# Kernel optimization log

Hardware: AMD Instinct MI355X
Metric: run time of the kernel (lower is better)

## Reference

```python
import jax, jax.numpy as jnp
import numpy as np

UNITS = 512
GROUPS = 32
EPS = 1e-5


def group_norm(x, w, b, groups=GROUPS, eps=EPS):
    B, C, H, W = x.shape
    xg = x.reshape(B, groups, C // groups, H, W)
    mean = xg.mean(axis=(2, 3, 4), keepdims=True)
    var = ((xg - mean) ** 2).mean(axis=(2, 3, 4), keepdims=True)
    xg = (xg - mean) * jax.lax.rsqrt(var + eps)
    return xg.reshape(B, C, H, W) * w[None, :, None, None] + b[None, :, None, None]


def conv1x1(x, w, b):
    # w: [out_ch, in_ch], b: [out_ch]
    return jnp.einsum('oc,bchw->bohw', w, x) + b[None, :, None, None]


def setup_inputs() -> dict:
    key = jax.random.key(0)
    ks = jax.random.split(key, 11)
    C = UNITS
    s = 1.0 / np.sqrt(C)
    return {
        'x': jax.random.normal(ks[0], (16, C, 64, 64), dtype=jnp.float32),
        'gn_w': jnp.ones((C,), dtype=jnp.float32),
        'gn_b': jnp.zeros((C,), dtype=jnp.float32),
        'wq': jax.random.normal(ks[1], (C, C), dtype=jnp.float32) * s,
        'bq': jnp.zeros((C,), dtype=jnp.float32),
        'wk': jax.random.normal(ks[2], (C, C), dtype=jnp.float32) * s,
        'bk': jnp.zeros((C,), dtype=jnp.float32),
        'wv': jax.random.normal(ks[3], (C, C), dtype=jnp.float32) * s,
        'bv': jnp.zeros((C,), dtype=jnp.float32),
        'wp': jax.random.normal(ks[4], (C, C), dtype=jnp.float32) * s,
        'bp': jnp.zeros((C,), dtype=jnp.float32),
    }


def reference(x, gn_w, gn_b, wq, bq, wk, bk, wv, bv, wp, bp):
    B, C, H, W = x.shape
    g = GROUPS
    xn = group_norm(x, gn_w, gn_b)
    q = conv1x1(xn, wq, bq).reshape(B, g, C // g, H * W)
    k = conv1x1(xn, wk, bk).reshape(B, g, C // g, H * W)
    v = conv1x1(xn, wv, bv).reshape(B, g, C // g, H * W)
    # channel attention: scores over per-group channel dims, spatial contracted
    attn = jnp.einsum('bgci,bgdi->bgcd', q, k) / jnp.sqrt(jnp.float32(C))
    attn = jax.nn.softmax(attn, axis=-1)
    out = jnp.einsum('bgcd,bgdi->bgci', attn, v).reshape(B, C, H, W)
    # NB: original adds proj(out) to out (not a residual to the input)
    return out + conv1x1(out, wp, bp)
```

## Files before the change

kernel.cpp:

```cpp
#include <hip/hip_runtime.h>

typedef __attribute__((ext_vector_type(8))) short bf16x8;
typedef __attribute__((ext_vector_type(4))) float f32x4;
typedef __attribute__((ext_vector_type(8))) unsigned short us8;
typedef unsigned short u16;
typedef unsigned int u32;

__device__ __forceinline__ u16 f2bf(float f){
  u32 u = __builtin_bit_cast(u32, f);
  u32 r = (u + 0x7fffu + ((u >> 16) & 1u)) >> 16;
  return (u16)r;
}

#define ASYNC_CP16(gp, lp) __builtin_amdgcn_global_load_lds( \
    (__attribute__((address_space(1))) void*)(gp), \
    (__attribute__((address_space(3))) void*)(lp), 16, 0, 0)

__device__ const int d_rt[10] = {0,0,0,0,1,1,1,2,2,3};
__device__ const int d_ct[10] = {0,1,2,3,1,2,3,2,3,3};

__global__ __launch_bounds__(256) void k_stats(const float* __restrict__ x,
    const float* __restrict__ gnw, const float* __restrict__ gnb,
    u16* __restrict__ xb, float* __restrict__ a, float* __restrict__ cv,
    float* __restrict__ sx)
{
  int b = blockIdx.x >> 5;
  int g = blockIdx.x & 31;
  int tid = threadIdx.x;
  int cl = tid >> 4;
  int l16 = tid & 15;
  int c = g * 16 + cl;
  const float* xp = x + ((long)(b * 512 + c)) * 4096;
  u16* xbp = xb + ((long)(b * 512 + c)) * 4096;
  float s = 0.f, sq = 0.f;
  for (int it = 0; it < 64; ++it) {
    int i4 = it * 16 + l16;
    float4 v = *(const float4*)(xp + i4 * 4);
    s  += v.x + v.y + v.z + v.w;
    sq += v.x * v.x + v.y * v.y + v.z * v.z + v.w * v.w;
    ushort4 o;
    o.x = f2bf(v.x); o.y = f2bf(v.y); o.z = f2bf(v.z); o.w = f2bf(v.w);
    *(ushort4*)(xbp + i4 * 4) = o;
  }
  for (int off = 8; off; off >>= 1) { s += __shfl_xor(s, off); sq += __shfl_xor(sq, off); }
  __shared__ float chS[16], chQ[16];
  if (l16 == 0) { chS[cl] = s; chQ[cl] = sq; }
  __syncthreads();
  if (tid < 16) {
    float S = 0.f, Q = 0.f;
    for (int j = 0; j < 16; ++j) { S += chS[j]; Q += chQ[j]; }
    float mean = S * (1.f / 65536.f);
    float var  = Q * (1.f / 65536.f) - mean * mean;
    float rs = rsqrtf(var + 1e-5f);
    int cc = g * 16 + tid;
    float av = gnw[cc] * rs;
    a[b * 512 + cc]  = av;
    cv[b * 512 + cc] = gnb[cc] - mean * av;
    sx[b * 512 + cc] = chS[tid];
  }
}

__global__ __launch_bounds__(256) void k_wconv(const float* __restrict__ wq,
    const float* __restrict__ wp, u16* __restrict__ wqb, u16* __restrict__ wpI)
{
  int i = blockIdx.x * 256 + threadIdx.x;
  wqb[i] = f2bf(wq[i]);
  float add = ((i >> 9) == (i & 511)) ? 1.f : 0.f;
  wpI[i] = f2bf(wp[i] + add);
}

__global__ __launch_bounds__(256) void k_transpose(const u16* __restrict__ xb,
                                                   u16* __restrict__ xT)
{
  __shared__ u16 t[64][72];
  int i0 = blockIdx.x * 64, e0 = blockIdx.y * 64, b = blockIdx.z;
  int tid = threadIdx.x;
  #pragma unroll
  for (int p = 0; p < 2; ++p) {
    int task = p * 256 + tid;
    int er = task >> 3, ic = (task & 7) * 8;
    us8 v = *(const us8*)(xb + ((long)(b * 512 + e0 + er)) * 4096 + i0 + ic);
    #pragma unroll
    for (int j = 0; j < 8; ++j) t[ic + j][er] = v[j];
  }
  __syncthreads();
  #pragma unroll
  for (int p = 0; p < 2; ++p) {
    int task = p * 256 + tid;
    int ir = task >> 3, ec = (task & 7) * 8;
    us8 w = *(const us8*)&t[ir][ec];
    *(us8*)(xT + ((long)(b * 4096 + i0 + ir)) * 512 + e0 + ec) = w;
  }
}

#define SWZ_RD(row16, chunk) ((((chunk) ^ ((row16) & 7)) << 3))

__global__ __launch_bounds__(256) void k_gram_split(const u16* __restrict__ xb,
                                                    float* __restrict__ part)
{
  __shared__ u16 As[2][128 * 64];
  __shared__ u16 Bs[2][128 * 64];
  const int tid = threadIdx.x;
  const int wave = tid >> 6, lane = tid & 63;
  const int tile = blockIdx.x % 10, split = blockIdx.x / 10;
  const int b = blockIdx.y;
  const int tm = d_rt[tile] * 128, tn = d_ct[tile] * 128;
  const u16* Xb = xb + (long)b * 512 * 4096;
  const int wm = (wave >> 1) << 6, wn = (wave & 1) << 6;
  const int l15 = lane & 15, l4 = lane >> 4;

  f32x4 acc[4][4];
  f32x4 z = {0.f, 0.f, 0.f, 0.f};
  #pragma unroll
  for (int fm = 0; fm < 4; ++fm)
    #pragma unroll
    for (int fn = 0; fn < 4; ++fn) acc[fm][fn] = z;

  const int qa = wave * 4;
  const int srow = lane >> 3;
  const int k0 = split * 1024;
  const int NT = 16;

  auto STAGE = [&](int buf, int kt) {
    #pragma unroll
    for (int j = 0; j < 4; ++j) {
      int q = qa + j;
      int row = q * 8 + srow;
      int gcol = kt + (((lane & 7) ^ (row & 7)) << 3);
      ASYNC_CP16(Xb + (long)(tm + row) * 4096 + gcol, &As[buf][q * 512]);
      ASYNC_CP16(Xb + (long)(tn + row) * 4096 + gcol, &Bs[buf][q * 512]);
    }
  };

  STAGE(0, k0);
  int cur = 0;
  for (int t = 0; t < NT; ++t) {
    if (t + 1 < NT) {
      STAGE(cur ^ 1, k0 + (t + 1) * 64);
      asm volatile("s_waitcnt vmcnt(8)" ::: "memory");
    } else {
      asm volatile("s_waitcnt vmcnt(0)" ::: "memory");
    }
    __builtin_amdgcn_s_barrier();
    __builtin_amdgcn_sched_barrier(0);
    #pragma unroll
    for (int kk = 0; kk < 2; ++kk) {
      bf16x8 af[4], bfr[4];
      #pragma unroll
      for (int f = 0; f < 4; ++f) {
        af[f]  = *(const bf16x8*)&As[cur][(wm + f * 16 + l15) * 64 +
                                          SWZ_RD(l15, l4 + kk * 4)];
        bfr[f] = *(const bf16x8*)&Bs[cur][(wn + f * 16 + l15) * 64 +
                                          SWZ_RD(l15, l4 + kk * 4)];
      }
      #pragma unroll
      for (int fm = 0; fm < 4; ++fm)
        #pragma unroll
        for (int fn = 0; fn < 4; ++fn)
          acc[fm][fn] = __builtin_amdgcn_mfma_f32_16x16x32_bf16(
              bfr[fn], af[fm], acc[fm][fn], 0, 0, 0);
    }
    __builtin_amdgcn_sched_barrier(0);
    __builtin_amdgcn_s_barrier();
    cur ^= 1;
  }

  float* pp = part + ((((long)split * 16 + b) * 10 + tile) << 14);
  #pragma unroll
  for (int fm = 0; fm < 4; ++fm) {
    const int row = wm + fm * 16 + l15;
    #pragma unroll
    for (int fn = 0; fn < 4; ++fn) {
      const int col = wn + fn * 16 + l4 * 4;
      *(f32x4*)&pp[row * 128 + col] = acc[fm][fn];
    }
  }
}

__global__ __launch_bounds__(512) void k_gram_reduce(
    const float* __restrict__ part, const float* __restrict__ a,
    u16* __restrict__ Gp)
{
  const int tile = blockIdx.x, b = blockIdx.y;
  const int tmt = d_rt[tile], tnt = d_ct[tile];
  const int tm = tmt * 128, tn = tnt * 128;
  const int tid = threadIdx.x;
  __shared__ u16 t[128][130];
  const float* p0 = part + (((long)b * 10 + tile) << 14);
  const long ss = (long)16 * 10 * 16384;
  u16* Gb = Gp + (long)b * 262144;
  const float acol = a[b * 512 + tn + (tid & 127)];
  for (int chunk = 0; chunk < 32; ++chunk) {
    int idx = chunk * 512 + tid;
    int row = idx >> 7, col = idx & 127;
    float v = p0[idx] + p0[idx + ss] + p0[idx + 2 * ss] + p0[idx + 3 * ss];
    v *= a[b * 512 + tm + row] * acol;
    u16 bf = f2bf(v);
    Gb[(tm + row) * 512 + tn + col] = bf;
    t[row][col] = bf;
  }
  if (tmt != tnt) {
    __syncthreads();
    for (int chunk = 0; chunk < 32; ++chunk) {
      int idx = chunk * 512 + tid;
      int row = idx >> 7, col = idx & 127;
      Gb[(tn + row) * 512 + tm + col] = t[col][row];
    }
  }
}

template<int EPI>
__global__ __launch_bounds__(256) void k_ntgemm64(
    const u16* __restrict__ A, long sA, int lda,
    const u16* __restrict__ B, long sB, int ldb,
    float* __restrict__ fout, long sF, int ldf,
    u16* __restrict__ bout, long sO, int ldo_,
    const float* __restrict__ ascale)
{
  __shared__ u16 As[2][64 * 64];
  __shared__ u16 Bs[2][64 * 64];
  const int tid = threadIdx.x;
  const int wave = tid >> 6, lane = tid & 63;
  const int b = blockIdx.y;
  const int tm = (blockIdx.x >> 3) * 64, tn = (blockIdx.x & 7) * 64;
  const u16* Ab = A + sA * b;
  const u16* Bb = B + sB * b;
  const int wm = (wave >> 1) << 5, wn = (wave & 1) << 5;
  const int l15 = lane & 15, l4 = lane >> 4;

  f32x4 acc[2][2];
  f32x4 z = {0.f, 0.f, 0.f, 0.f};
  #pragma unroll
  for (int fm = 0; fm < 2; ++fm)
    #pragma unroll
    for (int fn = 0; fn < 2; ++fn) acc[fm][fn] = z;

  const int qa = wave * 2;
  const int srow = lane >> 3;
  const int NT = 8;

  auto STAGE = [&](int buf, int kt) {
    #pragma unroll
    for (int j = 0; j < 2; ++j) {
      int q = qa + j;
      int row = q * 8 + srow;
      int gcol = kt + (((lane & 7) ^ (row & 7)) << 3);
      ASYNC_CP16(Ab + (long)(tm + row) * lda + gcol, &As[buf][q * 512]);
      ASYNC_CP16(Bb + (long)(tn + row) * ldb + gcol, &Bs[buf][q * 512]);
    }
  };

  STAGE(0, 0);
  int cur = 0;
  for (int t = 0; t < NT; ++t) {
    if (t + 1 < NT) {
      STAGE(cur ^ 1, (t + 1) * 64);
      asm volatile("s_waitcnt vmcnt(4)" ::: "memory");
    } else {
      asm volatile("s_waitcnt vmcnt(0)" ::: "memory");
    }
    __builtin_amdgcn_s_barrier();
    __builtin_amdgcn_sched_barrier(0);
    #pragma unroll
    for (int kk = 0; kk < 2; ++kk) {
      bf16x8 af[2], bfr[2];
      #pragma unroll
      for (int f = 0; f < 2; ++f) {
        af[f]  = *(const bf16x8*)&As[cur][(wm + f * 16 + l15) * 64 +
                                          SWZ_RD(l15, l4 + kk * 4)];
        bfr[f] = *(const bf16x8*)&Bs[cur][(wn + f * 16 + l15) * 64 +
                                          SWZ_RD(l15, l4 + kk * 4)];
      }
      #pragma unroll
      for (int fm = 0; fm < 2; ++fm)
        #pragma unroll
        for (int fn = 0; fn < 2; ++fn)
          acc[fm][fn] = __builtin_amdgcn_mfma_f32_16x16x32_bf16(
              bfr[fn], af[fm], acc[fm][fn], 0, 0, 0);
    }
    __builtin_amdgcn_sched_barrier(0);
    __builtin_amdgcn_s_barrier();
    cur ^= 1;
  }

  #pragma unroll
  for (int fm = 0; fm < 2; ++fm) {
    const int row = tm + wm + fm * 16 + l15;
    #pragma unroll
    for (int fn = 0; fn < 2; ++fn) {
      const int col = tn + wn + fn * 16 + l4 * 4;
      f32x4 v = acc[fm][fn];
      if (EPI == 1) {
        *(f32x4*)&fout[sF * b + (long)row * ldf + col] = v;
      } else {
        f32x4 sc = *(const f32x4*)&ascale[b * 512 + col];
        ushort4 o;
        o.x = f2bf(v[0] * sc[0]); o.y = f2bf(v[1] * sc[1]);
        o.z = f2bf(v[2] * sc[2]); o.w = f2bf(v[3] * sc[3]);
        *(ushort4*)&bout[sO * b + (long)row * ldo_ + col] = o;
      }
    }
  }
}

__global__ __launch_bounds__(512, 2) void k_final(
    const u16* __restrict__ W3, const u16* __restrict__ xT,
    const float* __restrict__ cadd, float* __restrict__ out)
{
  __shared__ u16 As[2][256 * 64];
  __shared__ u16 Bs[2][256 * 64];
  const int tid = threadIdx.x;
  const int wave = tid >> 6, lane = tid & 63;
  const int b = blockIdx.y;
  const int bxx = blockIdx.x;
  const int mi = (bxx >> 3) & 1;
  const int ni = (bxx & 7) | ((bxx >> 4) << 3);
  const int tm = mi * 256, tn = ni * 256;
  const u16* Ab = W3 + (long)b * 262144;
  const u16* Bb = xT + (long)b * 4096 * 512;
  const int wmA = (wave >> 2) * 128, wnB = (wave & 3) * 64;
  const int l15 = lane & 15, l4 = lane >> 4;

  f32x4 acc[8][4];
  f32x4 z = {0.f, 0.f, 0.f, 0.f};
  #pragma unroll
  for (int fm = 0; fm < 8; ++fm)
    #pragma unroll
    for (int fn = 0; fn < 4; ++fn) acc[fm][fn] = z;

  const int qa = wave * 4;
  const int srow = lane >> 3;
  const int NT = 8;

  auto STAGE = [&](int buf, int kt) {
    #pragma unroll
    for (int j = 0; j < 4; ++j) {
      int q = qa + j;
      int row = q * 8 + srow;
      int gcol = kt + (((lane & 7) ^ (row & 7)) << 3);
      ASYNC_CP16(Ab + (long)(tm + row) * 512 + gcol, &As[buf][q * 512]);
      ASYNC_CP16(Bb + (long)(tn + row) * 512 + gcol, &Bs[buf][q * 512]);
    }
  };

  STAGE(0, 0);
  int cur = 0;
  for (int t = 0; t < NT; ++t) {
    if (t + 1 < NT) {
      STAGE(cur ^ 1, (t + 1) * 64);
      asm volatile("s_waitcnt vmcnt(8)" ::: "memory");
    } else {
      asm volatile("s_waitcnt vmcnt(0)" ::: "memory");
    }
    __builtin_amdgcn_s_barrier();
    __builtin_amdgcn_sched_barrier(0);
    #pragma unroll
    for (int kk = 0; kk < 2; ++kk) {
      bf16x8 af[8], bfr[4];
      #pragma unroll
      for (int f = 0; f < 8; ++f)
        af[f]  = *(const bf16x8*)&As[cur][(wmA + f * 16 + l15) * 64 +
                                          SWZ_RD(l15, l4 + kk * 4)];
      #pragma unroll
      for (int f = 0; f < 4; ++f)
        bfr[f] = *(const bf16x8*)&Bs[cur][(wnB + f * 16 + l15) * 64 +
                                          SWZ_RD(l15, l4 + kk * 4)];
      #pragma unroll
      for (int fm = 0; fm < 8; ++fm)
        #pragma unroll
        for (int fn = 0; fn < 4; ++fn)
          acc[fm][fn] = __builtin_amdgcn_mfma_f32_16x16x32_bf16(
              bfr[fn], af[fm], acc[fm][fn], 0, 0, 0);
    }
    __builtin_amdgcn_sched_barrier(0);
    __builtin_amdgcn_s_barrier();
    cur ^= 1;
  }

  float* ob = out + (long)b * 512 * 4096;
  #pragma unroll
  for (int fm = 0; fm < 8; ++fm) {
    const int row = tm + wmA + fm * 16 + l15;
    const float ca = cadd[b * 512 + row];
    #pragma unroll
    for (int fn = 0; fn < 4; ++fn) {
      const int col = tn + wnB + fn * 16 + l4 * 4;
      f32x4 v = acc[fm][fn];
      v[0] += ca; v[1] += ca; v[2] += ca; v[3] += ca;
      *(f32x4*)&ob[(long)row * 4096 + col] = v;
    }
  }
}

__global__ __launch_bounds__(256) void k_vec(
    const float* __restrict__ wq, const float* __restrict__ bq,
    const float* __restrict__ wk, const float* __restrict__ bk,
    const float* __restrict__ wv, const float* __restrict__ bv,
    const float* __restrict__ a, const float* __restrict__ cv,
    const float* __restrict__ sx,
    float* __restrict__ eq, float* __restrict__ uq, float* __restrict__ ek,
    float* __restrict__ uk, float* __restrict__ hv)
{
  int b = blockIdx.x / 5, which = blockIdx.x % 5;
  __shared__ float vec[512];
  int tid = threadIdx.x;
  for (int i = tid; i < 512; i += 256)
    vec[i] = (which == 1 || which == 3) ? a[b * 512 + i] * sx[b * 512 + i]
                                        : cv[b * 512 + i];
  __syncthreads();
  const float* W = (which < 2) ? wq : (which < 4) ? wk : wv;
  const float* bias = (which == 0) ? bq : (which == 2) ? bk : (which == 4) ? bv : nullptr;
  float* outp = (which == 0) ? eq : (which == 1) ? uq : (which == 2) ? ek
              : (which == 3) ? uk : hv;
  for (int c = tid; c < 512; c += 256) {
    const float* wr = W + (long)c * 512;
    float s2 = 0.f;
    for (int e = 0; e < 512; e += 4) {
      float4 w4 = *(const float4*)(wr + e);
      s2 += w4.x * vec[e] + w4.y * vec[e + 1] + w4.z * vec[e + 2] + w4.w * vec[e + 3];
    }
    if (bias) s2 += bias[c];
    outp[b * 512 + c] = s2;
  }
}

__global__ __launch_bounds__(256) void k_scores(
    const float* __restrict__ P,
    const float* __restrict__ wk, const float* __restrict__ wv,
    const float* __restrict__ eq, const float* __restrict__ uq,
    const float* __restrict__ ek, const float* __restrict__ uk,
    const float* __restrict__ hv,
    u16* __restrict__ UT, float* __restrict__ oc)
{
  int b = blockIdx.x >> 5, g = blockIdx.x & 31;
  int tid = threadIdx.x;
  __shared__ float Pl[16 * 516];
  __shared__ float Wl[16 * 516];
  __shared__ float at[16][16];

  const float* Pb = P + (long)b * 262144 + g * 16 * 512;
  for (int t = tid; t < 16 * 128; t += 256) {
    int r = t >> 7, q = t & 127;
    *(float4*)&Pl[r * 516 + q * 4] = *(const float4*)(Pb + r * 512 + q * 4);
  }
  const float* Wkb = wk + (long)g * 16 * 512;
  for (int t = tid; t < 16 * 128; t += 256) {
    int r = t >> 7, q = t & 127;
    *(float4*)&Wl[r * 516 + q * 4] = *(const float4*)(Wkb + r * 512 + q * 4);
  }
  __syncthreads();

  int c = tid >> 4, d = tid & 15;
  float s0 = 0.f;
  for (int e = 0; e < 512; e += 4) {
    float4 p4 = *(const float4*)&Pl[c * 516 + e];
    float4 w4 = *(const float4*)&Wl[d * 516 + e];
    s0 += p4.x * w4.x + p4.y * w4.y + p4.z * w4.z + p4.w * w4.w;
  }
  float eqc = eq[b * 512 + g * 16 + c], uqc = uq[b * 512 + g * 16 + c];
  float ekd = ek[b * 512 + g * 16 + d], ukd = uk[b * 512 + g * 16 + d];
  float s = (s0 + eqc * ukd + uqc * ekd + 4096.f * eqc * ekd) * 0.04419417382415922f;
  float m = s;
  for (int off = 8; off; off >>= 1) m = fmaxf(m, __shfl_xor(m, off));
  float p = expf(s - m);
  float sum = p;
  for (int off = 8; off; off >>= 1) sum += __shfl_xor(sum, off);
  at[c][d] = p / sum;
  __syncthreads();

  const float* Wvb = wv + (long)g * 16 * 512;
  for (int t = tid; t < 16 * 128; t += 256) {
    int r = t >> 7, q = t & 127;
    *(float4*)&Wl[r * 516 + q * 4] = *(const float4*)(Wvb + r * 512 + q * 4);
  }
  __syncthreads();

  for (int t = 0; t < 32; ++t) {
    int flat = t * 256 + tid;
    int cc = flat >> 9, e = flat & 511;
    float a2 = 0.f;
    #pragma unroll
    for (int dd = 0; dd < 16; ++dd) a2 += at[cc][dd] * Wl[dd * 516 + e];
    Pl[cc * 516 + e] = a2;
  }
  if (tid < 16) {
    float o2 = 0.f;
    #pragma unroll
    for (int dd = 0; dd < 16; ++dd) o2 += at[tid][dd] * hv[b * 512 + g * 16 + dd];
    oc[b * 512 + g * 16 + tid] = o2;
  }
  __syncthreads();
  for (int t = 0; t < 32; ++t) {
    int flat = t * 256 + tid;
    int cc = flat & 15, e = flat >> 4;
    UT[(long)b * 262144 + e * 512 + g * 16 + cc] = f2bf(Pl[cc * 516 + e]);
  }
}

__global__ __launch_bounds__(256) void k_c3(const float* __restrict__ wp,
    const float* __restrict__ bp, const float* __restrict__ oc,
    float* __restrict__ c3)
{
  int b = blockIdx.x >> 1;
  int o = (blockIdx.x & 1) * 256 + threadIdx.x;
  __shared__ float ov[512];
  for (int i = threadIdx.x; i < 512; i += 256) ov[i] = oc[b * 512 + i];
  __syncthreads();
  const float* wr = wp + (long)o * 512;
  float s = 0.f;
  for (int e = 0; e < 512; e += 4) {
    float4 w4 = *(const float4*)(wr + e);
    s += w4.x * ov[e] + w4.y * ov[e + 1] + w4.z * ov[e + 2] + w4.w * ov[e + 3];
  }
  c3[b * 512 + o] = oc[b * 512 + o] + s + bp[o];
}

extern "C" void kernel_launch(void* const* d_in, const int* in_sizes, int n_in,
                              void* d_out, int out_size, void* d_ws, size_t ws_size,
                              hipStream_t stream)
{
  (void)in_sizes; (void)n_in; (void)out_size; (void)ws_size;
  const float* x   = (const float*)d_in[0];
  const float* gnw = (const float*)d_in[1];
  const float* gnb = (const float*)d_in[2];
  const float* wq  = (const float*)d_in[3];
  const float* bq  = (const float*)d_in[4];
  const float* wk  = (const float*)d_in[5];
  const float* bk  = (const float*)d_in[6];
  const float* wv  = (const float*)d_in[7];
  const float* bv  = (const float*)d_in[8];
  const float* wp  = (const float*)d_in[9];
  const float* bp  = (const float*)d_in[10];
  float* out = (float*)d_out;

  char* ws = (char*)d_ws;
  u16* xT  = (u16*)ws;  ws += (size_t)16 * 4096 * 512 * 2;
  u16* Gp  = (u16*)ws;  ws += (size_t)16 * 512 * 512 * 2;
  float* P = (float*)ws; ws += (size_t)16 * 512 * 512 * 4;
  u16* UT  = (u16*)ws;  ws += (size_t)16 * 512 * 512 * 2;
  u16* W3  = (u16*)ws;  ws += (size_t)16 * 512 * 512 * 2;
  u16* wqb = (u16*)ws;  ws += (size_t)512 * 512 * 2;
  u16* wpI = (u16*)ws;  ws += (size_t)512 * 512 * 2;
  float* a  = (float*)ws; ws += 16 * 512 * 4;
  float* cv = (float*)ws; ws += 16 * 512 * 4;
  float* sx = (float*)ws; ws += 16 * 512 * 4;
  float* eq = (float*)ws; ws += 16 * 512 * 4;
  float* uq = (float*)ws; ws += 16 * 512 * 4;
  float* ek = (float*)ws; ws += 16 * 512 * 4;
  float* uk = (float*)ws; ws += 16 * 512 * 4;
  float* hv = (float*)ws; ws += 16 * 512 * 4;
  float* oc = (float*)ws; ws += 16 * 512 * 4;
  float* c3 = (float*)ws; ws += 16 * 512 * 4;

  u16* xb = (u16*)d_out;
  float* part = (float*)xT;

  k_stats<<<512, 256, 0, stream>>>(x, gnw, gnb, xb, a, cv, sx);
  k_wconv<<<1024, 256, 0, stream>>>(wq, wp, wqb, wpI);
  k_gram_split<<<dim3(40, 16), 256, 0, stream>>>(xb, part);
  k_gram_reduce<<<dim3(10, 16), 512, 0, stream>>>(part, a, Gp);
  k_transpose<<<dim3(64, 8, 16), 256, 0, stream>>>(xb, xT);
  k_vec<<<80, 256, 0, stream>>>(wq, bq, wk, bk, wv, bv, a, cv, sx,
                                eq, uq, ek, uk, hv);
  k_ntgemm64<1><<<dim3(64, 16), 256, 0, stream>>>(
      wqb, 0, 512, Gp, 262144, 512,
      P, 262144, 512, nullptr, 0, 0, nullptr);
  k_scores<<<512, 256, 0, stream>>>(P, wk, wv, eq, uq, ek, uk, hv, UT, oc);
  k_c3<<<32, 256, 0, stream>>>(wp, bp, oc, c3);
  k_ntgemm64<2><<<dim3(64, 16), 256, 0, stream>>>(
      wpI, 0, 512, UT, 262144, 512,
      nullptr, 0, 0, W3, 262144, 512, a);
  k_final<<<dim3(32, 16), 512, 0, stream>>>(W3, xT, c3, out);
}
```

Measured before the change: 281.2 us.

## Fuse weight conversion into stats kernel and shrink gram K-tile to 32

Folds the weight bf16 conversion into extra blocks of the stats kernel, removing one launch. Halves the gram_split K tile from 64 to 32 with 32 iterations and a 4-way swizzle, cutting LDS use and possibly raising occupancy at the cost of more barriers per K. Moves the partial-sum buffer into the output buffer after xb instead of aliasing xT, so the transpose can no longer collide with it.

New measurement: 285.8 us. About the same (+1.6%).

```diff
diff --git a/kernel.cpp b/kernel.cpp
--- a/kernel.cpp
+++ b/kernel.cpp
@@ -21,12 +21,20 @@
 
 __global__ __launch_bounds__(256) void k_stats(const float* __restrict__ x,
     const float* __restrict__ gnw, const float* __restrict__ gnb,
-    u16* __restrict__ xb, float* __restrict__ a, float* __restrict__ cv,
-    float* __restrict__ sx)
-{
+    const float* __restrict__ wq, const float* __restrict__ wp,
+    u16* __restrict__ xb, u16* __restrict__ wqb, u16* __restrict__ wpI,
+    float* __restrict__ a, float* __restrict__ cv, float* __restrict__ sx)
+{
+  int tid = threadIdx.x;
+  if (blockIdx.x >= 512) {
+    int i = (blockIdx.x - 512) * 256 + tid;
+    wqb[i] = f2bf(wq[i]);
+    float add = ((i >> 9) == (i & 511)) ? 1.f : 0.f;
+    wpI[i] = f2bf(wp[i] + add);
+    return;
+  }
   int b = blockIdx.x >> 5;
   int g = blockIdx.x & 31;
-  int tid = threadIdx.x;
   int cl = tid >> 4;
   int l16 = tid & 15;
   int c = g * 16 + cl;
@@ -60,15 +68,6 @@
   }
 }
 
-__global__ __launch_bounds__(256) void k_wconv(const float* __restrict__ wq,
-    const float* __restrict__ wp, u16* __restrict__ wqb, u16* __restrict__ wpI)
-{
-  int i = blockIdx.x * 256 + threadIdx.x;
-  wqb[i] = f2bf(wq[i]);
-  float add = ((i >> 9) == (i & 511)) ? 1.f : 0.f;
-  wpI[i] = f2bf(wp[i] + add);
-}
-
 __global__ __launch_bounds__(256) void k_transpose(const u16* __restrict__ xb,
                                                    u16* __restrict__ xT)
 {
@@ -98,8 +97,8 @@
 __global__ __launch_bounds__(256) void k_gram_split(const u16* __restrict__ xb,
                                                     float* __restrict__ part)
 {
-  __shared__ u16 As[2][128 * 64];
-  __shared__ u16 Bs[2][128 * 64];
+  __shared__ u16 As[2][128 * 32];
+  __shared__ u16 Bs[2][128 * 32];
   const int tid = threadIdx.x;
   const int wave = tid >> 6, lane = tid & 63;
   const int tile = blockIdx.x % 10, split = blockIdx.x / 10;
@@ -116,50 +115,45 @@
     #pragma unroll
     for (int fn = 0; fn < 4; ++fn) acc[fm][fn] = z;
 
-  const int qa = wave * 4;
-  const int srow = lane >> 3;
   const int k0 = split * 1024;
-  const int NT = 16;
+  const int NT = 32;
 
   auto STAGE = [&](int buf, int kt) {
     #pragma unroll
-    for (int j = 0; j < 4; ++j) {
-      int q = qa + j;
-      int row = q * 8 + srow;
-      int gcol = kt + (((lane & 7) ^ (row & 7)) << 3);
-      ASYNC_CP16(Xb + (long)(tm + row) * 4096 + gcol, &As[buf][q * 512]);
-      ASYNC_CP16(Xb + (long)(tn + row) * 4096 + gcol, &Bs[buf][q * 512]);
+    for (int l = 0; l < 2; ++l) {
+      int fbase = l * 256 + wave * 64;
+      int flat  = fbase + lane;
+      int row = flat >> 2, cseg = flat & 3;
+      int gcol = kt + ((cseg ^ (row & 3)) << 3);
+      ASYNC_CP16(Xb + (long)(tm + row) * 4096 + gcol, &As[buf][fbase * 8]);
+      ASYNC_CP16(Xb + (long)(tn + row) * 4096 + gcol, &Bs[buf][fbase * 8]);
     }
   };
 
   STAGE(0, k0);
   int cur = 0;
+  const int rswz = (l4 ^ (l15 & 3)) << 3;
   for (int t = 0; t < NT; ++t) {
     if (t + 1 < NT) {
-      STAGE(cur ^ 1, k0 + (t + 1) * 64);
-      asm volatile("s_waitcnt vmcnt(8)" ::: "memory");
+      STAGE(cur ^ 1, k0 + (t + 1) * 32);
+      asm volatile("s_waitcnt vmcnt(4)" ::: "memory");
     } else {
       asm volatile("s_waitcnt vmcnt(0)" ::: "memory");
     }
     __builtin_amdgcn_s_barrier();
     __builtin_amdgcn_sched_barrier(0);
-    #pragma unroll
-    for (int kk = 0; kk < 2; ++kk) {
-      bf16x8 af[4], bfr[4];
+    bf16x8 af[4], bfr[4];
+    #pragma unroll
+    for (int f = 0; f < 4; ++f) {
+      af[f]  = *(const bf16x8*)&As[cur][(wm + f * 16 + l15) * 32 + rswz];
+      bfr[f] = *(const bf16x8*)&Bs[cur][(wn + f * 16 + l15) * 32 + rswz];
+    }
+    #pragma unroll
+    for (int fm = 0; fm < 4; ++fm)
       #pragma unroll
-      for (int f = 0; f < 4; ++f) {
-        af[f]  = *(const bf16x8*)&As[cur][(wm + f * 16 + l15) * 64 +
-                                          SWZ_RD(l15, l4 + kk * 4)];
-        bfr[f] = *(const bf16x8*)&Bs[cur][(wn + f * 16 + l15) * 64 +
-                                          SWZ_RD(l15, l4 + kk * 4)];
-      }
-      #pragma unroll
-      for (int fm = 0; fm < 4; ++fm)
-        #pragma unroll
-        for (int fn = 0; fn < 4; ++fn)
-          acc[fm][fn] = __builtin_amdgcn_mfma_f32_16x16x32_bf16(
-              bfr[fn], af[fm], acc[fm][fn], 0, 0, 0);
-    }
+      for (int fn = 0; fn < 4; ++fn)
+        acc[fm][fn] = __builtin_amdgcn_mfma_f32_16x16x32_bf16(
+            bfr[fn], af[fm], acc[fm][fn], 0, 0, 0);
     __builtin_amdgcn_sched_barrier(0);
     __builtin_amdgcn_s_barrier();
     cur ^= 1;
@@ -553,10 +547,10 @@
   float* c3 = (float*)ws; ws += 16 * 512 * 4;
 
   u16* xb = (u16*)d_out;
-  float* part = (float*)xT;
-
-  k_stats<<<512, 256, 0, stream>>>(x, gnw, gnb, xb, a, cv, sx);
-  k_wconv<<<1024, 256, 0, stream>>>(wq, wp, wqb, wpI);
+  float* part = (float*)((char*)d_out + 67108864);
+
+  k_stats<<<1536, 256, 0, stream>>>(x, gnw, gnb, wq, wp, xb, wqb, wpI,
+                                    a, cv, sx);
   k_gram_split<<<dim3(40, 16), 256, 0, stream>>>(xb, part);
   k_gram_reduce<<<dim3(10, 16), 512, 0, stream>>>(part, a, Gp);
   k_transpose<<<dim3(64, 8, 16), 256, 0, stream>>>(xb, xT);
```

## Retile final GEMM to 128x128 tiles and fold weight conversion into stats

Applied to the files above, without the earlier changes.

The final output GEMM changes from 256x256 tiles with 512 threads and 8x4 MFMA fragments per wave to 128x128 tiles with 256 threads and 4x4 fragments, launched as 2048 blocks instead of 512. The aim is finer-grained parallelism and lower register and LDS pressure per block, traded against less data reuse per tile and more global loads. Separately, the weight bf16-conversion kernel is merged into the group-norm stats kernel as extra blocks, removing one launch. The Gram partial-sum buffer is moved to the upper half of the output buffer instead of aliasing xT.

After: 285.6 us. No clear change (+1.5%).

```diff
diff --git a/kernel.cpp b/kernel.cpp
--- a/kernel.cpp
+++ b/kernel.cpp
@@ -21,12 +21,20 @@
 
 __global__ __launch_bounds__(256) void k_stats(const float* __restrict__ x,
     const float* __restrict__ gnw, const float* __restrict__ gnb,
-    u16* __restrict__ xb, float* __restrict__ a, float* __restrict__ cv,
-    float* __restrict__ sx)
-{
+    const float* __restrict__ wq, const float* __restrict__ wp,
+    u16* __restrict__ xb, u16* __restrict__ wqb, u16* __restrict__ wpI,
+    float* __restrict__ a, float* __restrict__ cv, float* __restrict__ sx)
+{
+  int tid = threadIdx.x;
+  if (blockIdx.x >= 512) {
+    int i = (blockIdx.x - 512) * 256 + tid;
+    wqb[i] = f2bf(wq[i]);
+    float add = ((i >> 9) == (i & 511)) ? 1.f : 0.f;
+    wpI[i] = f2bf(wp[i] + add);
+    return;
+  }
   int b = blockIdx.x >> 5;
   int g = blockIdx.x & 31;
-  int tid = threadIdx.x;
   int cl = tid >> 4;
   int l16 = tid & 15;
   int c = g * 16 + cl;
@@ -58,15 +66,6 @@
     cv[b * 512 + cc] = gnb[cc] - mean * av;
     sx[b * 512 + cc] = chS[tid];
   }
-}
-
-__global__ __launch_bounds__(256) void k_wconv(const float* __restrict__ wq,
-    const float* __restrict__ wp, u16* __restrict__ wqb, u16* __restrict__ wpI)
-{
-  int i = blockIdx.x * 256 + threadIdx.x;
-  wqb[i] = f2bf(wq[i]);
-  float add = ((i >> 9) == (i & 511)) ? 1.f : 0.f;
-  wpI[i] = f2bf(wp[i] + add);
 }
 
 __global__ __launch_bounds__(256) void k_transpose(const u16* __restrict__ xb,
@@ -303,28 +302,26 @@
   }
 }
 
-__global__ __launch_bounds__(512, 2) void k_final(
+__global__ __launch_bounds__(256) void k_final(
     const u16* __restrict__ W3, const u16* __restrict__ xT,
     const float* __restrict__ cadd, float* __restrict__ out)
 {
-  __shared__ u16 As[2][256 * 64];
-  __shared__ u16 Bs[2][256 * 64];
+  __shared__ u16 As[2][128 * 64];
+  __shared__ u16 Bs[2][128 * 64];
   const int tid = threadIdx.x;
   const int wave = tid >> 6, lane = tid & 63;
   const int b = blockIdx.y;
-  const int bxx = blockIdx.x;
-  const int mi = (bxx >> 3) & 1;
-  const int ni = (bxx & 7) | ((bxx >> 4) << 3);
-  const int tm = mi * 256, tn = ni * 256;
+  const int tm = (blockIdx.x >> 5) * 128;
+  const int tn = (blockIdx.x & 31) * 128;
   const u16* Ab = W3 + (long)b * 262144;
   const u16* Bb = xT + (long)b * 4096 * 512;
-  const int wmA = (wave >> 2) * 128, wnB = (wave & 3) * 64;
+  const int wm = (wave >> 1) << 6, wn = (wave & 1) << 6;
   const int l15 = lane & 15, l4 = lane >> 4;
 
-  f32x4 acc[8][4];
+  f32x4 acc[4][4];
   f32x4 z = {0.f, 0.f, 0.f, 0.f};
   #pragma unroll
-  for (int fm = 0; fm < 8; ++fm)
+  for (int fm = 0; fm < 4; ++fm)
     #pragma unroll
     for (int fn = 0; fn < 4; ++fn) acc[fm][fn] = z;
 
@@ -356,17 +353,16 @@
     __builtin_amdgcn_sched_barrier(0);
     #pragma unroll
     for (int kk = 0; kk < 2; ++kk) {
-      bf16x8 af[8], bfr[4];
+      bf16x8 af[4], bfr[4];
       #pragma unroll
-      for (int f = 0; f < 8; ++f)
-        af[f]  = *(const bf16x8*)&As[cur][(wmA + f * 16 + l15) * 64 +
+      for (int f = 0; f < 4; ++f) {
+        af[f]  = *(const bf16x8*)&As[cur][(wm + f * 16 + l15) * 64 +
                                           SWZ_RD(l15, l4 + kk * 4)];
+        bfr[f] = *(const bf16x8*)&Bs[cur][(wn + f * 16 + l15) * 64 +
+                                          SWZ_RD(l15, l4 + kk * 4)];
+      }
       #pragma unroll
-      for (int f = 0; f < 4; ++f)
-        bfr[f] = *(const bf16x8*)&Bs[cur][(wnB + f * 16 + l15) * 64 +
-                                          SWZ_RD(l15, l4 + kk * 4)];
-      #pragma unroll
-      for (int fm = 0; fm < 8; ++fm)
+      for (int fm = 0; fm < 4; ++fm)
         #pragma unroll
         for (int fn = 0; fn < 4; ++fn)
           acc[fm][fn] = __builtin_amdgcn_mfma_f32_16x16x32_bf16(
@@ -379,12 +375,12 @@
 
   float* ob = out + (long)b * 512 * 4096;
   #pragma unroll
-  for (int fm = 0; fm < 8; ++fm) {
-    const int row = tm + wmA + fm * 16 + l15;
+  for (int fm = 0; fm < 4; ++fm) {
+    const int row = tm + wm + fm * 16 + l15;
     const float ca = cadd[b * 512 + row];
     #pragma unroll
     for (int fn = 0; fn < 4; ++fn) {
-      const int col = tn + wnB + fn * 16 + l4 * 4;
+      const int col = tn + wn + fn * 16 + l4 * 4;
       f32x4 v = acc[fm][fn];
       v[0] += ca; v[1] += ca; v[2] += ca; v[3] += ca;
       *(f32x4*)&ob[(long)row * 4096 + col] = v;
@@ -553,10 +549,10 @@
   float* c3 = (float*)ws; ws += 16 * 512 * 4;
 
   u16* xb = (u16*)d_out;
-  float* part = (float*)xT;
-
-  k_stats<<<512, 256, 0, stream>>>(x, gnw, gnb, xb, a, cv, sx);
-  k_wconv<<<1024, 256, 0, stream>>>(wq, wp, wqb, wpI);
+  float* part = (float*)((char*)d_out + 67108864);
+
+  k_stats<<<1536, 256, 0, stream>>>(x, gnw, gnb, wq, wp, xb, wqb, wpI,
+                                    a, cv, sx);
   k_gram_split<<<dim3(40, 16), 256, 0, stream>>>(xb, part);
   k_gram_reduce<<<dim3(10, 16), 512, 0, stream>>>(part, a, Gp);
   k_transpose<<<dim3(64, 8, 16), 256, 0, stream>>>(xb, xT);
@@ -570,5 +566,5 @@
   k_ntgemm64<2><<<dim3(64, 16), 256, 0, stream>>>(
       wpI, 0, 512, UT, 262144, 512,
       nullptr, 0, 0, W3, 262144, 512, a);
-  k_final<<<dim3(32, 16), 512, 0, stream>>>(W3, xT, c3, out);
-}
+  k_final<<<dim3(128, 16), 256, 0, stream>>>(W3, xT, c3, out);
+}
```

## Merge gram split, transpose, vector and weight-convert kernels into one launch

Applied to the files above, without the earlier changes.

Four independent kernels (gram split GEMM, bf16 transpose, per-batch matrix-vector products, weight conversion) are combined into a single launch that dispatches on block index ranges. The aim is to remove three launch gaps and let the small memory-bound jobs fill the GPU alongside the 640 gram blocks instead of running serially. The gram partials buffer moves to a separate region of the output so it no longer aliases xT, which the transpose now writes at the same time. Every block now carries the gram kernel's large LDS allocation and register footprint, which may reduce occupancy for the light blocks.

Measured after the change: 264.3 us. -6.0%, faster.

```diff
diff --git a/kernel.cpp b/kernel.cpp
--- a/kernel.cpp
+++ b/kernel.cpp
@@ -60,50 +60,85 @@
   }
 }
 
-__global__ __launch_bounds__(256) void k_wconv(const float* __restrict__ wq,
-    const float* __restrict__ wp, u16* __restrict__ wqb, u16* __restrict__ wpI)
-{
-  int i = blockIdx.x * 256 + threadIdx.x;
-  wqb[i] = f2bf(wq[i]);
-  float add = ((i >> 9) == (i & 511)) ? 1.f : 0.f;
-  wpI[i] = f2bf(wp[i] + add);
-}
-
-__global__ __launch_bounds__(256) void k_transpose(const u16* __restrict__ xb,
-                                                   u16* __restrict__ xT)
-{
-  __shared__ u16 t[64][72];
-  int i0 = blockIdx.x * 64, e0 = blockIdx.y * 64, b = blockIdx.z;
-  int tid = threadIdx.x;
-  #pragma unroll
-  for (int p = 0; p < 2; ++p) {
-    int task = p * 256 + tid;
-    int er = task >> 3, ic = (task & 7) * 8;
-    us8 v = *(const us8*)(xb + ((long)(b * 512 + e0 + er)) * 4096 + i0 + ic);
-    #pragma unroll
-    for (int j = 0; j < 8; ++j) t[ic + j][er] = v[j];
-  }
-  __syncthreads();
-  #pragma unroll
-  for (int p = 0; p < 2; ++p) {
-    int task = p * 256 + tid;
-    int ir = task >> 3, ec = (task & 7) * 8;
-    us8 w = *(const us8*)&t[ir][ec];
-    *(us8*)(xT + ((long)(b * 4096 + i0 + ir)) * 512 + e0 + ec) = w;
-  }
-}
-
 #define SWZ_RD(row16, chunk) ((((chunk) ^ ((row16) & 7)) << 3))
 
-__global__ __launch_bounds__(256) void k_gram_split(const u16* __restrict__ xb,
-                                                    float* __restrict__ part)
+__global__ __launch_bounds__(256) void k_combo(const u16* __restrict__ xb,
+    float* __restrict__ part, u16* __restrict__ xT,
+    const float* __restrict__ wq, const float* __restrict__ bq,
+    const float* __restrict__ wk, const float* __restrict__ bk,
+    const float* __restrict__ wv, const float* __restrict__ bv,
+    const float* __restrict__ wp,
+    const float* __restrict__ a, const float* __restrict__ cv,
+    const float* __restrict__ sx,
+    u16* __restrict__ wqb, u16* __restrict__ wpI,
+    float* __restrict__ eq, float* __restrict__ uq, float* __restrict__ ek,
+    float* __restrict__ uk, float* __restrict__ hv)
 {
   __shared__ u16 As[2][128 * 64];
   __shared__ u16 Bs[2][128 * 64];
+  const int bid = blockIdx.x;
   const int tid = threadIdx.x;
+
+  if (bid >= 8912) {
+    int i = (bid - 8912) * 256 + tid;
+    wqb[i] = f2bf(wq[i]);
+    float add = ((i >> 9) == (i & 511)) ? 1.f : 0.f;
+    wpI[i] = f2bf(wp[i] + add);
+    return;
+  }
+
+  if (bid >= 8832) {
+    int v = bid - 8832;
+    int b = v / 5, which = v % 5;
+    float* vec = (float*)&As[0][0];
+    for (int i = tid; i < 512; i += 256)
+      vec[i] = (which == 1 || which == 3) ? a[b * 512 + i] * sx[b * 512 + i]
+                                          : cv[b * 512 + i];
+    __syncthreads();
+    const float* W = (which < 2) ? wq : (which < 4) ? wk : wv;
+    const float* bias = (which == 0) ? bq : (which == 2) ? bk
+                      : (which == 4) ? bv : nullptr;
+    float* outp = (which == 0) ? eq : (which == 1) ? uq : (which == 2) ? ek
+                : (which == 3) ? uk : hv;
+    for (int c = tid; c < 512; c += 256) {
+      const float* wr = W + (long)c * 512;
+      float s2 = 0.f;
+      for (int e = 0; e < 512; e += 4) {
+        float4 w4 = *(const float4*)(wr + e);
+        s2 += w4.x * vec[e] + w4.y * vec[e+1] + w4.z * vec[e+2] + w4.w * vec[e+3];
+      }
+      if (bias) s2 += bias[c];
+      outp[b * 512 + c] = s2;
+    }
+    return;
+  }
+
+  if (bid >= 640) {
+    int t = bid - 640;
+    int i0 = (t & 63) * 64, e0 = ((t >> 6) & 7) * 64, b = t >> 9;
+    u16 (*tl)[72] = (u16(*)[72])(&As[0][0]);
+    #pragma unroll
+    for (int p = 0; p < 2; ++p) {
+      int task = p * 256 + tid;
+      int er = task >> 3, ic = (task & 7) * 8;
+      us8 v = *(const us8*)(xb + ((long)(b * 512 + e0 + er)) * 4096 + i0 + ic);
+      #pragma unroll
+      for (int j = 0; j < 8; ++j) tl[ic + j][er] = v[j];
+    }
+    __syncthreads();
+    #pragma unroll
+    for (int p = 0; p < 2; ++p) {
+      int task = p * 256 + tid;
+      int ir = task >> 3, ec = (task & 7) * 8;
+      us8 w = *(const us8*)&tl[ir][ec];
+      *(us8*)(xT + ((long)(b * 4096 + i0 + ir)) * 512 + e0 + ec) = w;
+    }
+    return;
+  }
+
   const int wave = tid >> 6, lane = tid & 63;
-  const int tile = blockIdx.x % 10, split = blockIdx.x / 10;
-  const int b = blockIdx.y;
+  const int tile = bid % 10, split = (bid / 10) & 3;
+  const int b = bid / 40;
   const int tm = d_rt[tile] * 128, tn = d_ct[tile] * 128;
   const u16* Xb = xb + (long)b * 512 * 4096;
   const int wm = (wave >> 1) << 6, wn = (wave & 1) << 6;
@@ -389,38 +424,6 @@
       v[0] += ca; v[1] += ca; v[2] += ca; v[3] += ca;
       *(f32x4*)&ob[(long)row * 4096 + col] = v;
     }
-  }
-}
-
-__global__ __launch_bounds__(256) void k_vec(
-    const float* __restrict__ wq, const float* __restrict__ bq,
-    const float* __restrict__ wk, const float* __restrict__ bk,
-    const float* __restrict__ wv, const float* __restrict__ bv,
-    const float* __restrict__ a, const float* __restrict__ cv,
-    const float* __restrict__ sx,
-    float* __restrict__ eq, float* __restrict__ uq, float* __restrict__ ek,
-    float* __restrict__ uk, float* __restrict__ hv)
-{
-  int b = blockIdx.x / 5, which = blockIdx.x % 5;
-  __shared__ float vec[512];
-  int tid = threadIdx.x;
-  for (int i = tid; i < 512; i += 256)
-    vec[i] = (which == 1 || which == 3) ? a[b * 512 + i] * sx[b * 512 + i]
-                                        : cv[b * 512 + i];
-  __syncthreads();
-  const float* W = (which < 2) ? wq : (which < 4) ? wk : wv;
-  const float* bias = (which == 0) ? bq : (which == 2) ? bk : (which == 4) ? bv : nullptr;
-  float* outp = (which == 0) ? eq : (which == 1) ? uq : (which == 2) ? ek
-              : (which == 3) ? uk : hv;
-  for (int c = tid; c < 512; c += 256) {
-    const float* wr = W + (long)c * 512;
-    float s2 = 0.f;
-    for (int e = 0; e < 512; e += 4) {
-      float4 w4 = *(const float4*)(wr + e);
-      s2 += w4.x * vec[e] + w4.y * vec[e + 1] + w4.z * vec[e + 2] + w4.w * vec[e + 3];
-    }
-    if (bias) s2 += bias[c];
-    outp[b * 512 + c] = s2;
   }
 }
 
@@ -553,15 +556,14 @@
   float* c3 = (float*)ws; ws += 16 * 512 * 4;
 
   u16* xb = (u16*)d_out;
-  float* part = (float*)xT;
+  float* part = (float*)((char*)d_out + 67108864);
 
   k_stats<<<512, 256, 0, stream>>>(x, gnw, gnb, xb, a, cv, sx);
-  k_wconv<<<1024, 256, 0, stream>>>(wq, wp, wqb, wpI);
-  k_gram_split<<<dim3(40, 16), 256, 0, stream>>>(xb, part);
+  k_combo<<<9936, 256, 0, stream>>>(xb, part, xT,
+                                    wq, bq, wk, bk, wv, bv, wp,
+                                    a, cv, sx, wqb, wpI,
+                                    eq, uq, ek, uk, hv);
   k_gram_reduce<<<dim3(10, 16), 512, 0, stream>>>(part, a, Gp);
-  k_transpose<<<dim3(64, 8, 16), 256, 0, stream>>>(xb, xT);
-  k_vec<<<80, 256, 0, stream>>>(wq, bq, wk, bk, wv, bv, a, cv, sx,
-                                eq, uq, ek, uk, hv);
   k_ntgemm64<1><<<dim3(64, 16), 256, 0, stream>>>(
       wqb, 0, 512, Gp, 262144, 512,
       P, 262144, 512, nullptr, 0, 0, nullptr);
```
